# Optimization experiments

Measured on AMD Instinct MI355X. Metric: run time of the kernel, lower is better.

## Reference

```python
import jax, jax.numpy as jnp
import numpy as np

INPUT_SIZE = 608
STRIDE = 32
NUM_CLASSES = 20
NMS_THRESH = 0.5
NUM_ANCHOR = 5
ANCHORS = np.array([[1.19, 1.98], [2.79, 4.59], [4.53, 8.92], [8.06, 5.29], [10.32, 10.65]], dtype=np.float32)


def _conv(x, w, b, pad):
    # x: NCHW, w: OIHW
    y = jax.lax.conv_general_dilated(x, w, (1, 1), [(pad, pad), (pad, pad)],
                                     dimension_numbers=('NCHW', 'OIHW', 'NCHW'))
    return y + b[None, :, None, None]


def _leaky(x):
    return jnp.where(x > 0, x, 0.1 * x)


def _reorg(x, s=2):
    # space-to-depth, darknet reorg: [B,C,H,W] -> [B,C*s*s,H/s,W/s]
    B, C, H, W = x.shape
    x = x.reshape(B, C, H // s, s, W // s, s)
    x = x.transpose(0, 3, 5, 1, 2, 4)
    return x.reshape(B, C * s * s, H // s, W // s)


def _forward_boxes_scores(feat_layer2, feat_layer3, w1a, b1a, w1b, b1b, wr, br, w2, b2, wp, bp):
    p5 = _leaky(_conv(feat_layer3, w1a, b1a, 1))
    p5 = _leaky(_conv(p5, w1b, b1b, 1))
    p4 = _reorg(_leaky(_conv(feat_layer2, wr, br, 0)))         # [1,256,19,19]
    p5 = jnp.concatenate([p4, p5], axis=1)                      # [1,1280,19,19]
    p5 = _leaky(_conv(p5, w2, b2, 1))
    pred = _conv(p5, wp, bp, 0)                                 # [1,125,19,19]
    B, C, H, W = pred.shape
    pred = pred.transpose(0, 2, 3, 1).reshape(B, H * W, C)
    conf = pred[:, :, :NUM_ANCHOR].reshape(B, H * W * NUM_ANCHOR, 1)
    cls = pred[:, :, NUM_ANCHOR:(1 + NUM_CLASSES) * NUM_ANCHOR].reshape(B, H * W * NUM_ANCHOR, NUM_CLASSES)
    reg = pred[:, :, (1 + NUM_CLASSES) * NUM_ANCHOR:].reshape(B, H * W, NUM_ANCHOR, 4)
    # decode_xywh
    gy, gx = jnp.meshgrid(jnp.arange(H), jnp.arange(W), indexing='ij')
    grid = jnp.stack([gx, gy], axis=-1).astype(pred.dtype).reshape(1, H * W, 1, 2)
    anchor_wh = jnp.asarray(ANCHORS).reshape(1, 1, NUM_ANCHOR, 2)
    xy = jax.nn.sigmoid(reg[..., :2]) + grid
    wh = jnp.exp(reg[..., 2:]) * anchor_wh
    xywh = jnp.concatenate([xy, wh], axis=-1).reshape(B, -1, 4) * STRIDE
    boxes = jnp.concatenate([xywh[..., :2] - 0.5 * xywh[..., 2:],
                             xywh[..., :2] + 0.5 * xywh[..., 2:]], axis=-1)
    boxes = jnp.clip(boxes[0] / INPUT_SIZE, 0.0, 1.0)           # [N,4]
    scores = jax.nn.sigmoid(conf[0]) * jax.nn.softmax(cls[0], axis=-1)  # [N,20]
    return boxes, scores


def _per_class_nms(boxes, scores, class_mask):
    # greedy sequential NMS, faithful to the torch while-loop (suppress iff IoU > thresh)
    N = boxes.shape[0]
    s = jnp.where(class_mask, scores, -jnp.inf)
    order = jnp.argsort(-s)
    b = boxes[order]
    valid = class_mask[order]
    x1, y1, x2, y2 = b[:, 0], b[:, 1], b[:, 2], b[:, 3]
    areas = (x2 - x1) * (y2 - y1)
    iw = jnp.maximum(1e-10, jnp.minimum(x2[:, None], x2[None, :]) - jnp.maximum(x1[:, None], x1[None, :]))
    ih = jnp.maximum(1e-10, jnp.minimum(y2[:, None], y2[None, :]) - jnp.maximum(y1[:, None], y1[None, :]))
    inter = iw * ih
    iou = inter / (areas[:, None] + areas[None, :] - inter)
    upper = jnp.arange(N)[None, :] > jnp.arange(N)[:, None]
    sup_mat = (iou > NMS_THRESH) & upper

    def body(i, state):
        suppressed, keep = state
        cur = valid[i] & jnp.logical_not(suppressed[i])
        keep = keep.at[i].set(cur)
        suppressed = suppressed | (cur & sup_mat[i])
        return suppressed, keep

    _, keep_sorted = jax.lax.fori_loop(0, N, body, (jnp.zeros(N, bool), jnp.zeros(N, bool)))
    return jnp.zeros(N, bool).at[order].set(keep_sorted)


def setup_inputs() -> dict:
    key = jax.random.key(0)
    ks = jax.random.split(key, 8)
    w = lambda k, shape: jax.random.normal(k, shape, jnp.float32) * 0.01
    return {
        'feat_layer2': jax.random.normal(ks[0], (1, 512, 38, 38), jnp.float32),
        'feat_layer3': jax.random.normal(ks[1], (1, 1024, 19, 19), jnp.float32),
        'w1a': w(ks[2], (1024, 1024, 3, 3)), 'b1a': jnp.zeros((1024,), jnp.float32),
        'w1b': w(ks[3], (1024, 1024, 3, 3)), 'b1b': jnp.zeros((1024,), jnp.float32),
        'wr': w(ks[4], (64, 512, 1, 1)), 'br': jnp.zeros((64,), jnp.float32),
        'w2': w(ks[5], (1024, 1280, 3, 3)), 'b2': jnp.zeros((1024,), jnp.float32),
        'wp': w(ks[6], (125, 1024, 1, 1)), 'bp': jnp.zeros((125,), jnp.float32),
    }


def reference(feat_layer2, feat_layer3, w1a, b1a, w1b, b1b, wr, br, w2, b2, wp, bp):
    boxes, scores_full = _forward_boxes_scores(feat_layer2, feat_layer3,
                                               w1a, b1a, w1b, b1b, wr, br, w2, b2, wp, bp)
    cls_inds = jnp.argmax(scores_full, axis=1)                          # [N]
    scores = jnp.take_along_axis(scores_full, cls_inds[:, None], axis=1)[:, 0]
    masks = cls_inds[None, :] == jnp.arange(NUM_CLASSES)[:, None]       # [20,N]
    keeps = jax.vmap(lambda m: _per_class_nms(boxes, scores, m))(masks)
    keep = jnp.any(keeps, axis=0)                                       # [N] bool, fixed-shape mask
    return boxes, scores, cls_inds, keep
```

## Files before the change

kernel.cpp:

```cpp
#include <hip/hip_runtime.h>

typedef _Float16 f16;
typedef _Float16 f16x8 __attribute__((ext_vector_type(8)));
typedef float f32x4 __attribute__((ext_vector_type(4)));

#define N_BOX 1805
#define NPIX 361
#define NCLS 20
#define GNW 29
#define MB_ROWS 226

__device__ __forceinline__ float leakyf(float x){ return x > 0.f ? x : 0.1f*x; }
__device__ __forceinline__ float sigmoidf_(float x){ return 1.f/(1.f + expf(-x)); }

__global__ void transpose_k(const float* __restrict__ src, float* __restrict__ dst, int R, int C){
  int i = blockIdx.x*256 + threadIdx.x;
  if (i < R*C){ int r = i / C, c = i % C; dst[c*R + r] = src[i]; }
}

__global__ void wprep9_k(const float* __restrict__ w, f16* __restrict__ wpk,
                         int Cin, int cpt, int NK, int total){
  int gid = blockIdx.x*256 + threadIdx.x;
  if (gid >= total) return;
  int jci  = gid & 3;
  int rest = gid >> 2;
  int nblk = Cin >> 5;
  int ciblk = rest % nblk;
  int co    = rest / nblk;
  int cob = co >> 7, row = co & 127;
  const float* src = w + ((size_t)co*Cin + ciblk*32 + jci*8)*9;
  float v[72];
  #pragma unroll
  for (int q = 0; q < 72; ++q) v[q] = src[q];
  int rx = row & 7;
  #pragma unroll
  for (int t = 0; t < 9; ++t){
    f16x8 hv, lv;
    #pragma unroll
    for (int k = 0; k < 8; ++k){
      float f = v[k*9 + t] * 64.f;
      f16 hi = (f16)f;
      hv[k] = hi;
      lv[k] = (f16)(f - (float)hi);
    }
    size_t tb = ((size_t)cob*NK + t*cpt + ciblk)*8192 + row*64;
    *(f16x8*)(wpk + tb + ((0*4 + jci) ^ rx)*8) = hv;
    *(f16x8*)(wpk + tb + ((1*4 + jci) ^ rx)*8) = lv;
  }
}

__global__ void act1prep_k(const float* __restrict__ feat3, f16* __restrict__ ah, f16* __restrict__ al){
  int i = blockIdx.x*256 + threadIdx.x;
  if (i >= NPIX*1024) return;
  int p = i >> 10, c = i & 1023;
  float v = feat3[c*NPIX + p];
  f16 hi = (f16)v; f16 lo = (f16)(v - (float)hi);
  ah[i] = hi; al[i] = lo;
}

__global__ __launch_bounds__(256) void reorg_conv_k(const float* __restrict__ feat2,
    const float* __restrict__ wrT, const float* __restrict__ br,
    f16* __restrict__ cath, f16* __restrict__ catl){
  int c  = threadIdx.x & 63;
  int pq = threadIdx.x >> 6;
  int pix = blockIdx.x*4 + pq;
  int y = pix / 38, x = pix % 38;
  __shared__ float s_in[64][4];
  float acc = br[c];
  for (int cb = 0; cb < 512; cb += 64){
    __syncthreads();
    { int k = threadIdx.x >> 2, pp = threadIdx.x & 3;
      s_in[k][pp] = feat2[(cb + k)*1444 + blockIdx.x*4 + pp]; }
    __syncthreads();
    #pragma unroll
    for (int k = 0; k < 64; ++k)
      acc = fmaf(wrT[(cb+k)*64 + c], s_in[k][pq], acc);
  }
  float v = leakyf(acc);
  int co = ((y & 1)*2 + (x & 1))*64 + c;
  int p = (y>>1)*19 + (x>>1);
  f16 hi = (f16)v; f16 lo = (f16)(v - (float)hi);
  size_t o = (size_t)p*1280 + co;
  cath[o] = hi; catl[o] = lo;
}

__global__ __launch_bounds__(256) void conv_mfma_k(
    const f16* __restrict__ wpk,
    const f16* __restrict__ ahi, const f16* __restrict__ alo,
    float* __restrict__ part, int Cin, int chunks, int cpt, int NK)
{
  int cob = blockIdx.x;
  int px0 = blockIdx.y * 128;
  int ks  = blockIdx.z;
  int kc0 = ks * chunks;
  int tid = threadIdx.x;

  __shared__ f16 sA[2][128*64];

  const f16* wbase = wpk + ((size_t)cob*NK + kc0)*8192;
  int aost[4];
  #pragma unroll
  for (int j = 0; j < 4; ++j) aost[j] = (tid + j*256)*8;

  int lane = tid & 63, wid = tid >> 6;
  int lrow = lane & 15, lgrp = lane >> 4;
  int wr = wid >> 1, wc = wid & 1;
  int aoffH[4], aoffL[4];
  #pragma unroll
  for (int m = 0; m < 4; ++m){
    int rA = wr*64 + m*16 + lrow;
    aoffH[m] = (rA*128 + lgrp*16)     ^ ((rA & 7) << 4);
    aoffL[m] = (rA*128 + (4+lgrp)*16) ^ ((rA & 7) << 4);
  }
  int bpy[4], bpx[4]; bool bpv[4];
  #pragma unroll
  for (int n = 0; n < 4; ++n){
    int p = px0 + wc*64 + n*16 + lrow;
    bpv[n] = (p < NPIX);
    int pc = bpv[n] ? p : 0;
    bpy[n] = pc / 19; bpx[n] = pc - bpy[n]*19;
  }

  f32x4 acc[4][4] = {};
  f16x8 sa0, sa1, sa2, sa3;

  auto LOADA = [&](int i){
    const f16* as = wbase + (size_t)i*8192;
    sa0 = *(const f16x8*)(as + aost[0]);
    sa1 = *(const f16x8*)(as + aost[1]);
    sa2 = *(const f16x8*)(as + aost[2]);
    sa3 = *(const f16x8*)(as + aost[3]);
  };
  auto WRITEA = [&](int buf){
    *(f16x8*)(&sA[buf][aost[0]]) = sa0;
    *(f16x8*)(&sA[buf][aost[1]]) = sa1;
    *(f16x8*)(&sA[buf][aost[2]]) = sa2;
    *(f16x8*)(&sA[buf][aost[3]]) = sa3;
  };

  LOADA(0);
  WRITEA(0);
  __syncthreads();

  for (int i = 0; i < chunks; ++i){
    int kc = kc0 + i;
    int t = kc / cpt;
    int ci0 = (kc - t*cpt) * 32;
    int dy = t/3, dx = t - dy*3;

    f16x8 bh[4], bl[4];
    #pragma unroll
    for (int n = 0; n < 4; ++n){
      int yy = bpy[n] + dy - 1, xx = bpx[n] + dx - 1;
      bool ok = bpv[n] & ((unsigned)yy < 19u) & ((unsigned)xx < 19u);
      f16x8 z = {};
      bh[n] = z; bl[n] = z;
      if (ok){
        size_t bo = (size_t)(yy*19 + xx)*Cin + ci0 + lgrp*8;
        bh[n] = *(const f16x8*)(ahi + bo);
        bl[n] = *(const f16x8*)(alo + bo);
      }
    }

    int cur = i & 1;
    bool more = (i + 1 < chunks);
    if (more) LOADA(i + 1);

    #pragma unroll
    for (int m = 0; m < 4; ++m){
      f16x8 ah = *(const f16x8*)((char*)sA[cur] + aoffH[m]);
      f16x8 al = *(const f16x8*)((char*)sA[cur] + aoffL[m]);
      #pragma unroll
      for (int n = 0; n < 4; ++n){
        acc[m][n] = __builtin_amdgcn_mfma_f32_16x16x32_f16(ah, bh[n], acc[m][n], 0,0,0);
        acc[m][n] = __builtin_amdgcn_mfma_f32_16x16x32_f16(ah, bl[n], acc[m][n], 0,0,0);
        acc[m][n] = __builtin_amdgcn_mfma_f32_16x16x32_f16(al, bh[n], acc[m][n], 0,0,0);
      }
    }
    if (more) WRITEA(cur ^ 1);
    __syncthreads();
  }

  #pragma unroll
  for (int m = 0; m < 4; ++m){
    #pragma unroll
    for (int n = 0; n < 4; ++n){
      int pp = px0 + wc*64 + n*16 + lrow;
      if (pp < NPIX){
        int co = cob*128 + wr*64 + m*16 + lgrp*4;
        size_t base = ((size_t)ks*1024 + co)*NPIX + pp;
        part[base          ] = acc[m][n][0];
        part[base +   NPIX ] = acc[m][n][1];
        part[base + 2*NPIX ] = acc[m][n][2];
        part[base + 3*NPIX ] = acc[m][n][3];
      }
    }
  }
}

__global__ void reduce16v_k(const float* __restrict__ part, const float* __restrict__ bias,
                            f16* __restrict__ dhi, f16* __restrict__ dlo,
                            int Cstride, int Coff, int splitk){
  int i = blockIdx.x*256 + threadIdx.x;
  if (i >= 1024*NPIX) return;
  int co = i / NPIX, p = i - co*NPIX;
  float s = 0.f;
  for (int k = 0; k < splitk; ++k) s += part[(size_t)k*1024*NPIX + i];
  float v = leakyf(s*0.015625f + bias[co]);
  f16 hi = (f16)v;
  f16 lo = (f16)(v - (float)hi);
  size_t o = (size_t)p*Cstride + Coff + co;
  dhi[o] = hi; dlo[o] = lo;
}

__global__ __launch_bounds__(256) void pred_conv_k(const f16* __restrict__ a3h, const f16* __restrict__ a3l,
    const float* __restrict__ wpT, const float* __restrict__ bp, float* __restrict__ pred){
  int c = threadIdx.x & 127, ph = threadIdx.x >> 7;
  int pix = blockIdx.x*2 + ph;
  __shared__ float s_in[64][2];
  float acc = 0.f;
  for (int cb = 0; cb < 1024; cb += 64){
    __syncthreads();
    if (threadIdx.x < 128){
      int k = threadIdx.x & 63, pp = threadIdx.x >> 6;
      int px2 = blockIdx.x*2 + pp;
      float v = 0.f;
      if (px2 < NPIX){
        size_t o = (size_t)px2*1024 + cb + k;
        v = (float)a3h[o] + (float)a3l[o];
      }
      s_in[k][pp] = v;
    }
    __syncthreads();
    if (c < 125){
      #pragma unroll
      for (int k = 0; k < 64; ++k)
        acc = fmaf(wpT[(cb+k)*125 + c], s_in[k][ph], acc);
    }
  }
  if (c < 125 && pix < NPIX) pred[c*NPIX + pix] = acc + bp[c];
}

__device__ const float ANCW[5] = {1.19f, 2.79f, 4.53f, 8.06f, 10.32f};
__device__ const float ANCH_[5] = {1.98f, 4.59f, 8.92f, 5.29f, 10.65f};

__global__ void decode_k(const float* __restrict__ pred, float* __restrict__ out,
                         int* __restrict__ cls_i, int* __restrict__ cnt){
  int n = blockIdx.x*256 + threadIdx.x;
  if (blockIdx.x == 0 && threadIdx.x < NCLS) cnt[threadIdx.x] = 0;
  if (n >= N_BOX) return;
  int p = n / 5, a = n % 5;
  float conf = pred[a*NPIX + p];
  float cl[20]; float m = -1e30f;
  #pragma unroll
  for (int k = 0; k < 20; ++k){ cl[k] = pred[(5 + a*20 + k)*NPIX + p]; m = fmaxf(m, cl[k]); }
  float s = 0.f;
  #pragma unroll
  for (int k = 0; k < 20; ++k){ cl[k] = expf(cl[k]-m); s += cl[k]; }
  int bi = 0; float bv = cl[0];
  #pragma unroll
  for (int k = 1; k < 20; ++k) if (cl[k] > bv){ bv = cl[k]; bi = k; }
  float score = sigmoidf_(conf) * (bv / s);
  float tx = pred[(105 + a*4 + 0)*NPIX + p];
  float ty = pred[(105 + a*4 + 1)*NPIX + p];
  float tw = pred[(105 + a*4 + 2)*NPIX + p];
  float th = pred[(105 + a*4 + 3)*NPIX + p];
  float gx = (float)(p % 19), gy = (float)(p / 19);
  float cx = (sigmoidf_(tx) + gx) * 32.f;
  float cy = (sigmoidf_(ty) + gy) * 32.f;
  float bw = expf(tw) * ANCW[a] * 32.f;
  float bh = expf(th) * ANCH_[a] * 32.f;
  float x1 = fminf(fmaxf((cx - 0.5f*bw) / 608.f, 0.f), 1.f);
  float y1 = fminf(fmaxf((cy - 0.5f*bh) / 608.f, 0.f), 1.f);
  float x2 = fminf(fmaxf((cx + 0.5f*bw) / 608.f, 0.f), 1.f);
  float y2 = fminf(fmaxf((cy + 0.5f*bh) / 608.f, 0.f), 1.f);
  out[n*4+0]=x1; out[n*4+1]=y1; out[n*4+2]=x2; out[n*4+3]=y2;
  out[7220 + n]  = score;
  out[9025 + n]  = (float)bi;
  out[10830 + n] = 0.f;
  cls_i[n] = bi;
}

__global__ __launch_bounds__(256) void rank_k(const float* __restrict__ scores,
    const int* __restrict__ cls_i, int* __restrict__ ord, int* __restrict__ cnt){
  __shared__ float s_sc[N_BOX];
  __shared__ short s_cl[N_BOX];
  int tid = threadIdx.x;
  for (int j = tid; j < N_BOX; j += 256){ s_sc[j] = scores[j]; s_cl[j] = (short)cls_i[j]; }
  __syncthreads();
  int wid = tid >> 6, lane = tid & 63;
  int i = blockIdx.x*4 + wid;
  if (i >= N_BOX) return;
  float si = s_sc[i]; short ci = s_cl[i];
  int r = 0;
  for (int j = lane; j < N_BOX; j += 64){
    float sj = s_sc[j];
    r += (int)((s_cl[j] == ci) & ((sj > si) | ((sj == si) & (j < i))));
  }
  #pragma unroll
  for (int o = 32; o; o >>= 1) r += __shfl_down(r, o);
  if (lane == 0){
    ord[ci*N_BOX + r] = i;
    atomicAdd(&cnt[ci], 1);
  }
}

__global__ __launch_bounds__(256) void maskbuild_k(const float* __restrict__ boxes,
    const int* __restrict__ ord, const int* __restrict__ cnt,
    unsigned long long* __restrict__ gmask){
  __shared__ float X1[N_BOX], Y1[N_BOX], X2[N_BOX], Y2[N_BOX], AR[N_BOX];
  int c = blockIdx.x, chunk = blockIdx.y, tid = threadIdx.x;
  int n = cnt[c];
  int r0 = chunk*MB_ROWS;
  if (n <= 0 || r0 >= n) return;
  int r1 = r0 + MB_ROWS; if (r1 > n) r1 = n;
  int rows_here = r1 - r0;
  for (int t = tid; t < n; t += 256){
    int bi = ord[c*N_BOX + t];
    float x1 = boxes[bi*4+0], y1 = boxes[bi*4+1], x2 = boxes[bi*4+2], y2 = boxes[bi*4+3];
    X1[t]=x1; Y1[t]=y1; X2[t]=x2; Y2[t]=y2; AR[t]=(x2-x1)*(y2-y1);
  }
  __syncthreads();
  int nw = (n + 63) >> 6;
  unsigned long long* rows = gmask + (size_t)c*N_BOX*GNW;
  for (int task = tid; task < rows_here*nw; task += 256){
    int w = task / rows_here, ri = task - w*rows_here;
    int i = r0 + ri;
    float ax1=X1[i], ay1=Y1[i], ax2=X2[i], ay2=Y2[i], areaA=AR[i];
    unsigned long long bits = 0;
    int j0 = w << 6;
    int jb = i+1 > j0 ? i+1 : j0;
    int je = j0+64 < n ? j0+64 : n;
    for (int j = jb; j < je; ++j){
      float iw = fmaxf(1e-10f, fminf(ax2,X2[j]) - fmaxf(ax1,X1[j]));
      float ih = fmaxf(1e-10f, fminf(ay2,Y2[j]) - fmaxf(ay1,Y1[j]));
      float inter = iw*ih;
      float iou = inter / (areaA + AR[j] - inter);
      bits |= (unsigned long long)(iou > 0.5f) << (j - j0);
    }
    rows[(size_t)i*GNW + w] = bits;
  }
}

__global__ __launch_bounds__(64) void nmsscan_k(const int* __restrict__ ord,
    const int* __restrict__ cnt, const unsigned long long* __restrict__ gmask,
    float* __restrict__ keep){
  __shared__ int sidx[N_BOX];
  int c = blockIdx.x, lane = threadIdx.x;
  int n = cnt[c];
  if (n <= 0) return;
  int nw = (n + 63) >> 6;
  for (int t = lane; t < n; t += 64) sidx[t] = ord[c*N_BOX + t];
  __syncthreads();
  const unsigned long long* rows = gmask + (size_t)c*N_BOX*GNW;
  bool act = lane < nw;
  unsigned long long S = 0;
  unsigned long long diag = (lane < n) ? rows[(size_t)lane*GNW + 0] : 0ull;
  for (int w = 0; w < nw; ++w){
    int base = w << 6;
    int nb = n - base; if (nb > 64) nb = 64;
    unsigned int slo = (unsigned)__builtin_amdgcn_readlane((int)(unsigned)S, w);
    unsigned int shi = (unsigned)__builtin_amdgcn_readlane((int)(unsigned)(S >> 32), w);
    unsigned long long sup = ((unsigned long long)shi << 32) | slo;
    unsigned long long validm = (nb >= 64) ? ~0ull : ((1ull << nb) - 1ull);
    unsigned long long avail = ~sup & validm;
    unsigned long long kmask = 0;
    unsigned long long diag_next = 0;
    if (w+1 < nw){
      int i2 = base + 64 + lane;
      if (i2 < n) diag_next = rows[(size_t)i2*GNW + (w+1)];
    }
    while (avail){
      int b = __builtin_ctzll(avail);
      kmask |= 1ull << b;
      unsigned int dlo = (unsigned)__builtin_amdgcn_readlane((int)(unsigned)diag, b);
      unsigned int dhi = (unsigned)__builtin_amdgcn_readlane((int)(unsigned)(diag >> 32), b);
      unsigned long long drow = ((unsigned long long)dhi << 32) | dlo;
      sup |= drow;
      avail &= ~(1ull << b);
      avail &= ~sup;
      if (act && lane > w)
        S |= rows[(size_t)(base + b)*GNW + lane];
    }
    if ((kmask >> lane) & 1ull) keep[sidx[base + lane]] = 1.f;
    diag = diag_next;
  }
}

static inline size_t align256(size_t x){ return (x + 255) & ~(size_t)255; }

extern "C" void kernel_launch(void* const* d_in, const int* in_sizes, int n_in,
                              void* d_out, int out_size, void* d_ws, size_t ws_size,
                              hipStream_t stream){
  const float* feat2 = (const float*)d_in[0];
  const float* feat3 = (const float*)d_in[1];
  const float* w1a = (const float*)d_in[2];
  const float* b1a = (const float*)d_in[3];
  const float* w1b = (const float*)d_in[4];
  const float* b1b = (const float*)d_in[5];
  const float* wr  = (const float*)d_in[6];
  const float* br  = (const float*)d_in[7];
  const float* w2  = (const float*)d_in[8];
  const float* b2  = (const float*)d_in[9];
  const float* wp  = (const float*)d_in[10];
  const float* bp  = (const float*)d_in[11];
  float* out = (float*)d_out;
  char* ws = (char*)d_ws;

  size_t off = 0;
  float* part = (float*)(ws + off); off = align256(off + (size_t)24*1024*NPIX*4);
  f16* wpk  = (f16*)(ws + off); off = align256(off + (size_t)8*360*8192*2);
  f16* a1h  = (f16*)(ws + off); off = align256(off + (size_t)NPIX*1024*2);
  f16* a1l  = (f16*)(ws + off); off = align256(off + (size_t)NPIX*1024*2);
  f16* a2h  = (f16*)(ws + off); off = align256(off + (size_t)NPIX*1024*2);
  f16* a2l  = (f16*)(ws + off); off = align256(off + (size_t)NPIX*1024*2);
  f16* a3h  = (f16*)(ws + off); off = align256(off + (size_t)NPIX*1024*2);
  f16* a3l  = (f16*)(ws + off); off = align256(off + (size_t)NPIX*1024*2);
  f16* cath = (f16*)(ws + off); off = align256(off + (size_t)NPIX*1280*2);
  f16* catl = (f16*)(ws + off); off = align256(off + (size_t)NPIX*1280*2);
  float* pred = (float*)(ws + off); off = align256(off + (size_t)125*NPIX*4);
  float* wrT  = (float*)(ws + off); off = align256(off + (size_t)512*64*4);
  float* wpT  = (float*)(ws + off); off = align256(off + (size_t)1024*125*4);
  int* cls_i  = (int*)(ws + off); off = align256(off + (size_t)N_BOX*4);
  int* ord    = (int*)(ws + off); off = align256(off + (size_t)NCLS*N_BOX*4);
  int* cnt    = (int*)(ws + off); off = align256(off + (size_t)NCLS*4);
  unsigned long long* gmask = (unsigned long long*)part;

  transpose_k<<<(64*512 + 255)/256, 256, 0, stream>>>(wr, wrT, 64, 512);
  transpose_k<<<(125*1024 + 255)/256, 256, 0, stream>>>(wp, wpT, 125, 1024);
  act1prep_k<<<(NPIX*1024 + 255)/256, 256, 0, stream>>>(feat3, a1h, a1l);
  reorg_conv_k<<<361, 256, 0, stream>>>(feat2, wrT, br, cath, catl);

  wprep9_k<<<(1024*32*4 + 255)/256, 256, 0, stream>>>(w1a, wpk, 1024, 32, 288, 1024*32*4);
  { dim3 g(8, 3, 16);
    conv_mfma_k<<<g, 256, 0, stream>>>(wpk, a1h, a1l, part, 1024, 18, 32, 288); }
  reduce16v_k<<<(1024*NPIX + 255)/256, 256, 0, stream>>>(part, b1a, a2h, a2l, 1024, 0, 16);

  wprep9_k<<<(1024*32*4 + 255)/256, 256, 0, stream>>>(w1b, wpk, 1024, 32, 288, 1024*32*4);
  { dim3 g(8, 3, 16);
    conv_mfma_k<<<g, 256, 0, stream>>>(wpk, a2h, a2l, part, 1024, 18, 32, 288); }
  reduce16v_k<<<(1024*NPIX + 255)/256, 256, 0, stream>>>(part, b1b, cath, catl, 1280, 256, 16);

  wprep9_k<<<(1024*40*4 + 255)/256, 256, 0, stream>>>(w2, wpk, 1280, 40, 360, 1024*40*4);
  { dim3 g(8, 3, 18);
    conv_mfma_k<<<g, 256, 0, stream>>>(wpk, cath, catl, part, 1280, 20, 40, 360); }
  reduce16v_k<<<(1024*NPIX + 255)/256, 256, 0, stream>>>(part, b2, a3h, a3l, 1024, 0, 18);

  pred_conv_k<<<181, 256, 0, stream>>>(a3h, a3l, wpT, bp, pred);
  decode_k<<<8, 256, 0, stream>>>(pred, out, cls_i, cnt);
  rank_k<<<(N_BOX + 3)/4, 256, 0, stream>>>(out + 7220, cls_i, ord, cnt);
  { dim3 mg(NCLS, 8);
    maskbuild_k<<<mg, 256, 0, stream>>>(out, ord, cnt, gmask); }
  nmsscan_k<<<NCLS, 64, 0, stream>>>(ord, cnt, gmask, out + 10830);
}
```

Measured before the change: 377.7 us.

## Stage activations in LDS and read pre-swizzled weights directly from global

The weight prep kernel now writes weights in a fragment-ready order, so each wave loads its MFMA A operands straight from global memory without going through LDS. The im2col activation tile is staged in double-buffered LDS instead, which lets the four waves share it rather than each issuing redundant gathers. The split-K factor also rises to 24 for all three convs, giving more blocks at the cost of larger partial buffers and more work in the reduce step. Reading weights directly from global depends on cache hits and may expose memory latency.

```diff
diff --git a/kernel.cpp b/kernel.cpp
--- a/kernel.cpp
+++ b/kernel.cpp
@@ -27,12 +27,14 @@
   int nblk = Cin >> 5;
   int ciblk = rest % nblk;
   int co    = rest / nblk;
-  int cob = co >> 7, row = co & 127;
   const float* src = w + ((size_t)co*Cin + ciblk*32 + jci*8)*9;
   float v[72];
   #pragma unroll
   for (int q = 0; q < 72; ++q) v[q] = src[q];
-  int rx = row & 7;
+  int rA = co & 127, cob = co >> 7;
+  int wr = rA >> 6, m = (rA >> 4) & 3, lrow = rA & 15;
+  size_t slotbase = (size_t)(wr*64 + jci*16 + lrow)*8;
+  f16x8* dst = (f16x8*)wpk;
   #pragma unroll
   for (int t = 0; t < 9; ++t){
     f16x8 hv, lv;
@@ -43,9 +45,9 @@
       hv[k] = hi;
       lv[k] = (f16)(f - (float)hi);
     }
-    size_t tb = ((size_t)cob*NK + t*cpt + ciblk)*8192 + row*64;
-    *(f16x8*)(wpk + tb + ((0*4 + jci) ^ rx)*8) = hv;
-    *(f16x8*)(wpk + tb + ((1*4 + jci) ^ rx)*8) = lv;
+    size_t tb = ((size_t)cob*NK + t*cpt + ciblk)*1024;
+    dst[tb + slotbase + m]     = hv;
+    dst[tb + slotbase + 4 + m] = lv;
   }
 }
 
@@ -95,89 +97,92 @@
   int kc0 = ks * chunks;
   int tid = threadIdx.x;
 
-  __shared__ f16 sA[2][128*64];
-
-  const f16* wbase = wpk + ((size_t)cob*NK + kc0)*8192;
-  int aost[4];
-  #pragma unroll
-  for (int j = 0; j < 4; ++j) aost[j] = (tid + j*256)*8;
+  __shared__ f16 sB[2][128*64];
 
   int lane = tid & 63, wid = tid >> 6;
   int lrow = lane & 15, lgrp = lane >> 4;
   int wr = wid >> 1, wc = wid & 1;
-  int aoffH[4], aoffL[4];
-  #pragma unroll
-  for (int m = 0; m < 4; ++m){
-    int rA = wr*64 + m*16 + lrow;
-    aoffH[m] = (rA*128 + lgrp*16)     ^ ((rA & 7) << 4);
-    aoffL[m] = (rA*128 + (4+lgrp)*16) ^ ((rA & 7) << 4);
-  }
-  int bpy[4], bpx[4]; bool bpv[4];
+
+  const f16x8* abase = (const f16x8*)wpk + (size_t)(cob*NK + kc0)*1024 + (size_t)(wr*64 + lane)*8;
+
+  int srow = tid >> 3;
+  int sdata = (tid & 7) ^ (srow & 7);
+  int sh = sdata >> 2, sjci = sdata & 3;
+  const f16* bbase = sh ? alo : ahi;
+  int spy[4], spx[4]; bool spv[4];
+  #pragma unroll
+  for (int s = 0; s < 4; ++s){
+    int p = px0 + srow + s*32;
+    spv[s] = (p < NPIX);
+    int pc = spv[s] ? p : 0;
+    spy[s] = pc / 19; spx[s] = pc - spy[s]*19;
+  }
+
+  int boffH[4], boffL[4];
   #pragma unroll
   for (int n = 0; n < 4; ++n){
-    int p = px0 + wc*64 + n*16 + lrow;
-    bpv[n] = (p < NPIX);
-    int pc = bpv[n] ? p : 0;
-    bpy[n] = pc / 19; bpx[n] = pc - bpy[n]*19;
+    int rB = wc*64 + n*16 + lrow;
+    boffH[n] = (rB*128 + lgrp*16)     ^ ((rB & 7) << 4);
+    boffL[n] = (rB*128 + (4+lgrp)*16) ^ ((rB & 7) << 4);
   }
 
   f32x4 acc[4][4] = {};
-  f16x8 sa0, sa1, sa2, sa3;
-
-  auto LOADA = [&](int i){
-    const f16* as = wbase + (size_t)i*8192;
-    sa0 = *(const f16x8*)(as + aost[0]);
-    sa1 = *(const f16x8*)(as + aost[1]);
-    sa2 = *(const f16x8*)(as + aost[2]);
-    sa3 = *(const f16x8*)(as + aost[3]);
-  };
-  auto WRITEA = [&](int buf){
-    *(f16x8*)(&sA[buf][aost[0]]) = sa0;
-    *(f16x8*)(&sA[buf][aost[1]]) = sa1;
-    *(f16x8*)(&sA[buf][aost[2]]) = sa2;
-    *(f16x8*)(&sA[buf][aost[3]]) = sa3;
-  };
-
-  LOADA(0);
-  WRITEA(0);
-  __syncthreads();
-
-  for (int i = 0; i < chunks; ++i){
+  f16x8 bs0, bs1, bs2, bs3;
+
+  auto LOADB = [&](int i){
     int kc = kc0 + i;
     int t = kc / cpt;
     int ci0 = (kc - t*cpt) * 32;
     int dy = t/3, dx = t - dy*3;
-
-    f16x8 bh[4], bl[4];
-    #pragma unroll
-    for (int n = 0; n < 4; ++n){
-      int yy = bpy[n] + dy - 1, xx = bpx[n] + dx - 1;
-      bool ok = bpv[n] & ((unsigned)yy < 19u) & ((unsigned)xx < 19u);
-      f16x8 z = {};
-      bh[n] = z; bl[n] = z;
+    f16x8 z = {};
+    bs0 = z; bs1 = z; bs2 = z; bs3 = z;
+    #pragma unroll
+    for (int s = 0; s < 4; ++s){
+      int yy = spy[s] + dy - 1, xx = spx[s] + dx - 1;
+      bool ok = spv[s] & ((unsigned)yy < 19u) & ((unsigned)xx < 19u);
       if (ok){
-        size_t bo = (size_t)(yy*19 + xx)*Cin + ci0 + lgrp*8;
-        bh[n] = *(const f16x8*)(ahi + bo);
-        bl[n] = *(const f16x8*)(alo + bo);
+        f16x8 vv = *(const f16x8*)(bbase + (size_t)(yy*19+xx)*Cin + ci0 + sjci*8);
+        if (s == 0) bs0 = vv; else if (s == 1) bs1 = vv; else if (s == 2) bs2 = vv; else bs3 = vv;
       }
     }
-
+  };
+  auto WRITEB = [&](int buf){
+    *(f16x8*)(&sB[buf][(tid +   0)*8]) = bs0;
+    *(f16x8*)(&sB[buf][(tid + 256)*8]) = bs1;
+    *(f16x8*)(&sB[buf][(tid + 512)*8]) = bs2;
+    *(f16x8*)(&sB[buf][(tid + 768)*8]) = bs3;
+  };
+
+  LOADB(0);
+  WRITEB(0);
+  __syncthreads();
+
+  for (int i = 0; i < chunks; ++i){
     int cur = i & 1;
     bool more = (i + 1 < chunks);
-    if (more) LOADA(i + 1);
+    if (more) LOADB(i + 1);
+
+    f16x8 bh[4], bl[4];
+    #pragma unroll
+    for (int n = 0; n < 4; ++n){
+      bh[n] = *(const f16x8*)((char*)sB[cur] + boffH[n]);
+      bl[n] = *(const f16x8*)((char*)sB[cur] + boffL[n]);
+    }
+    const f16x8* ap = abase + (size_t)i*1024;
+    f16x8 ahf[4], alf[4];
+    #pragma unroll
+    for (int m = 0; m < 4; ++m){ ahf[m] = ap[m]; alf[m] = ap[4+m]; }
 
     #pragma unroll
     for (int m = 0; m < 4; ++m){
-      f16x8 ah = *(const f16x8*)((char*)sA[cur] + aoffH[m]);
-      f16x8 al = *(const f16x8*)((char*)sA[cur] + aoffL[m]);
       #pragma unroll
       for (int n = 0; n < 4; ++n){
-        acc[m][n] = __builtin_amdgcn_mfma_f32_16x16x32_f16(ah, bh[n], acc[m][n], 0,0,0);
-        acc[m][n] = __builtin_amdgcn_mfma_f32_16x16x32_f16(ah, bl[n], acc[m][n], 0,0,0);
-        acc[m][n] = __builtin_amdgcn_mfma_f32_16x16x32_f16(al, bh[n], acc[m][n], 0,0,0);
+        acc[m][n] = __builtin_amdgcn_mfma_f32_16x16x32_f16(ahf[m], bh[n], acc[m][n], 0,0,0);
+        acc[m][n] = __builtin_amdgcn_mfma_f32_16x16x32_f16(ahf[m], bl[n], acc[m][n], 0,0,0);
+        acc[m][n] = __builtin_amdgcn_mfma_f32_16x16x32_f16(alf[m], bh[n], acc[m][n], 0,0,0);
       }
     }
-    if (more) WRITEA(cur ^ 1);
+    if (more) WRITEB(cur ^ 1);
     __syncthreads();
   }
 
@@ -432,19 +437,19 @@
   reorg_conv_k<<<361, 256, 0, stream>>>(feat2, wrT, br, cath, catl);
 
   wprep9_k<<<(1024*32*4 + 255)/256, 256, 0, stream>>>(w1a, wpk, 1024, 32, 288, 1024*32*4);
-  { dim3 g(8, 3, 16);
-    conv_mfma_k<<<g, 256, 0, stream>>>(wpk, a1h, a1l, part, 1024, 18, 32, 288); }
-  reduce16v_k<<<(1024*NPIX + 255)/256, 256, 0, stream>>>(part, b1a, a2h, a2l, 1024, 0, 16);
+  { dim3 g(8, 3, 24);
+    conv_mfma_k<<<g, 256, 0, stream>>>(wpk, a1h, a1l, part, 1024, 12, 32, 288); }
+  reduce16v_k<<<(1024*NPIX + 255)/256, 256, 0, stream>>>(part, b1a, a2h, a2l, 1024, 0, 24);
 
   wprep9_k<<<(1024*32*4 + 255)/256, 256, 0, stream>>>(w1b, wpk, 1024, 32, 288, 1024*32*4);
-  { dim3 g(8, 3, 16);
-    conv_mfma_k<<<g, 256, 0, stream>>>(wpk, a2h, a2l, part, 1024, 18, 32, 288); }
-  reduce16v_k<<<(1024*NPIX + 255)/256, 256, 0, stream>>>(part, b1b, cath, catl, 1280, 256, 16);
+  { dim3 g(8, 3, 24);
+    conv_mfma_k<<<g, 256, 0, stream>>>(wpk, a2h, a2l, part, 1024, 12, 32, 288); }
+  reduce16v_k<<<(1024*NPIX + 255)/256, 256, 0, stream>>>(part, b1b, cath, catl, 1280, 256, 24);
 
   wprep9_k<<<(1024*40*4 + 255)/256, 256, 0, stream>>>(w2, wpk, 1280, 40, 360, 1024*40*4);
-  { dim3 g(8, 3, 18);
-    conv_mfma_k<<<g, 256, 0, stream>>>(wpk, cath, catl, part, 1280, 20, 40, 360); }
-  reduce16v_k<<<(1024*NPIX + 255)/256, 256, 0, stream>>>(part, b2, a3h, a3l, 1024, 0, 18);
+  { dim3 g(8, 3, 24);
+    conv_mfma_k<<<g, 256, 0, stream>>>(wpk, cath, catl, part, 1280, 15, 40, 360); }
+  reduce16v_k<<<(1024*NPIX + 255)/256, 256, 0, stream>>>(part, b2, a3h, a3l, 1024, 0, 24);
 
   pred_conv_k<<<181, 256, 0, stream>>>(a3h, a3l, wpT, bp, pred);
   decode_k<<<8, 256, 0, stream>>>(pred, out, cls_i, cnt);
```

New measurement: 448.3 us. 1.19x slower.
